# Optimization experiments

Measured on AMD Instinct MI355X. Metric: run time of the kernel, lower is better.

Reference implementation:

```python
import jax, jax.numpy as jnp
import numpy as np
import math

D_MODEL = 1024
N_HEADS = 16
D_HEAD = D_MODEL // N_HEADS

def setup_inputs() -> dict:
    key = jax.random.key(0)
    k1, k2, k3 = jax.random.split(key, 3)
    x = jax.random.normal(k1, (4, 2048, D_MODEL), dtype=jnp.float32)
    # torch Linear weights are [out, in]; kept in that layout, applied as x @ W.T
    s = 1.0 / math.sqrt(D_MODEL)
    W_qkv = jax.random.uniform(k2, (3 * D_MODEL, D_MODEL), jnp.float32, -s, s)
    W_proj = jax.random.uniform(k3, (D_MODEL, D_MODEL), jnp.float32, -s, s)
    return {"x": x, "W_qkv": W_qkv, "W_proj": W_proj}

def reference(x, W_qkv, W_proj):
    B, T, d = x.shape
    qkv = x @ W_qkv.T  # [B,T,3d]
    q, k, v = jnp.split(qkv, 3, axis=-1)
    def split(t):
        return t.reshape(B, T, N_HEADS, D_HEAD).transpose(0, 2, 1, 3)  # [B,H,T,Dh]
    q, k, v = split(q), split(k), split(v)
    scores = jnp.einsum('bhqd,bhkd->bhqk', q, k) / math.sqrt(D_HEAD)
    mask = jnp.tril(jnp.ones((T, T), dtype=bool))
    scores = jnp.where(mask, scores, -jnp.inf)
    attn = jax.nn.softmax(scores, axis=-1)
    out = jnp.einsum('bhqk,bhkd->bhqd', attn, v)  # [B,H,T,Dh]
    out = out.transpose(0, 2, 1, 3).reshape(B, T, d)
    return out @ W_proj.T
```

## Files before the change

kernel.cpp:

```cpp
#include <hip/hip_runtime.h>
#include <hip/hip_bf16.h>
#include <math.h>

typedef __attribute__((ext_vector_type(8))) short short8;
typedef __attribute__((ext_vector_type(4))) float f32x4;
typedef __attribute__((ext_vector_type(16))) float f32x16;
typedef __attribute__((ext_vector_type(2))) unsigned uint2v;
typedef __attribute__((ext_vector_type(4))) unsigned uint4v;

#define B_  4
#define T_  2048
#define DM  1024
#define NH  16
#define DH  64
#define BH  (B_*NH)
#define M_  (B_*T_)

#define QSCALE 0.18033688011112042f

static __device__ __forceinline__ short f2bf(float f) {
  unsigned u = __float_as_uint(f);
  unsigned r = (u + 0x7fff + ((u >> 16) & 1)) >> 16;
  return (short)r;
}

static __device__ __forceinline__ unsigned cvtpk(float lo, float hi) {
  unsigned r;
  asm("v_cvt_pk_bf16_f32 %0, %1, %2" : "=v"(r) : "v"(lo), "v"(hi));
  return r;
}

static __device__ __forceinline__ float expasm(float x) {
  float r;
  asm("v_exp_f32 %0, %1" : "=v"(r) : "v"(x));
  return r;
}

static __device__ __forceinline__ void gload_lds16(const void* g, void* l) {
  __builtin_amdgcn_global_load_lds((const __attribute__((address_space(1))) void*)g,
                                   (__attribute__((address_space(3))) void*)l, 16, 0, 0);
}

__global__ void k_cvt3(const float4* __restrict__ x, const float4* __restrict__ wq,
                       const float4* __restrict__ wp, ushort4* __restrict__ ox,
                       ushort4* __restrict__ oq, ushort4* __restrict__ op) {
  const int n1 = M_ * DM / 4, n2 = 3 * DM * DM / 4, n3 = DM * DM / 4;
  int i = blockIdx.x * 256 + threadIdx.x;
  const float4* src;
  ushort4* dst;
  int j = i;
  if (i < n1) { src = x; dst = ox; }
  else if (i < n1 + n2) { src = wq; dst = oq; j = i - n1; }
  else if (i < n1 + n2 + n3) { src = wp; dst = op; j = i - n1 - n2; }
  else return;
  float4 v = src[j];
  ushort4 o;
  o.x = (ushort)f2bf(v.x); o.y = (ushort)f2bf(v.y);
  o.z = (ushort)f2bf(v.z); o.w = (ushort)f2bf(v.w);
  dst[j] = o;
}

#define GEMM_STAGE(SRCA, SRCB, dA, dB, m0_, n0_, k0_)                          \
  {                                                                            \
    _Pragma("unroll")                                                          \
    for (int i = 0; i < 4; ++i) {                                              \
      int lin = i * 256 + tid;                                                 \
      int row = lin >> 3, pseg = lin & 7;                                      \
      int gseg = pseg ^ (row & 7);                                             \
      gload_lds16(&SRCA[(size_t)((m0_) + row) * DM + (k0_) + gseg * 8],        \
                  &(dA)[lin * 8]);                                             \
    }                                                                          \
    _Pragma("unroll")                                                          \
    for (int i = 0; i < 4; ++i) {                                              \
      int lin = i * 256 + tid;                                                 \
      int row = lin >> 3, pseg = lin & 7;                                      \
      int gseg = pseg ^ (row & 7);                                             \
      gload_lds16(&SRCB[(size_t)((n0_) + row) * DM + (k0_) + gseg * 8],        \
                  &(dB)[lin * 8]);                                             \
    }                                                                          \
  }

#define GEMM_COMPUTE(pA, pB)                                                   \
  {                                                                            \
    _Pragma("unroll")                                                          \
    for (int kk = 0; kk < 2; ++kk) {                                           \
      short8 aF[4], bF[4];                                                     \
      _Pragma("unroll")                                                        \
      for (int m = 0; m < 4; ++m)                                              \
        aF[m] = *(const short8*)&(pA)[(wr * 64 + m * 16 + fr) * 64 +           \
                                      (((kk * 4 + fq) ^ (fr & 7)) * 8)];       \
      _Pragma("unroll")                                                        \
      for (int n = 0; n < 4; ++n)                                              \
        bF[n] = *(const short8*)&(pB)[(wc * 64 + n * 16 + fr) * 64 +           \
                                      (((kk * 4 + fq) ^ (fr & 7)) * 8)];       \
      __builtin_amdgcn_s_setprio(1);                                           \
      _Pragma("unroll")                                                        \
      for (int m = 0; m < 4; ++m)                                              \
        _Pragma("unroll")                                                      \
        for (int n = 0; n < 4; ++n)                                            \
          acc[m][n] = __builtin_amdgcn_mfma_f32_16x16x32_bf16(aF[m], bF[n],    \
                                                              acc[m][n], 0, 0, 0); \
      __builtin_amdgcn_s_setprio(0);                                           \
    }                                                                          \
  }

#define GEMM_KLOOP(SRCA, SRCB, m0_, n0_)                                       \
  GEMM_STAGE(SRCA, SRCB, sA0, sB0, m0_, n0_, 0);                               \
  {                                                                            \
    _Pragma("unroll 1")                                                        \
    for (int t = 0; t < 16; ++t) {                                             \
      short* pA = (t & 1) ? sA1 : sA0;                                         \
      short* pB = (t & 1) ? sB1 : sB0;                                         \
      if (t < 15) {                                                            \
        short* nA = (t & 1) ? sA0 : sA1;                                       \
        short* nB = (t & 1) ? sB0 : sB1;                                       \
        GEMM_STAGE(SRCA, SRCB, nA, nB, m0_, n0_, (t + 1) * 64);                \
        asm volatile("s_waitcnt vmcnt(8)" ::: "memory");                       \
      } else {                                                                 \
        asm volatile("s_waitcnt vmcnt(0)" ::: "memory");                       \
      }                                                                        \
      __builtin_amdgcn_s_barrier();                                            \
      __builtin_amdgcn_sched_barrier(0);                                       \
      GEMM_COMPUTE(pA, pB);                                                    \
      asm volatile("" ::: "memory");                                           \
      __builtin_amdgcn_s_barrier();                                            \
    }                                                                          \
  }

__global__ __launch_bounds__(256, 2) void k_gemm_qkv(
    const short* __restrict__ A,
    const short* __restrict__ W,
    short* __restrict__ Qb, short* __restrict__ Kb, short* __restrict__ Vtb) {
  const int tid = threadIdx.x;
  const int w = tid >> 6, l = tid & 63;
  const int wr = w >> 1, wc = w & 1;
  const int fq = l >> 4, fr = l & 15;
  const int m0 = blockIdx.x * 128;
  const int n0 = blockIdx.y * 128;

  __shared__ short lds[32768];
  short* sA0 = lds;
  short* sA1 = lds + 8192;
  short* sB0 = lds + 16384;
  short* sB1 = lds + 24576;

  f32x4 acc[4][4] = {};
  GEMM_KLOOP(A, W, m0, n0);
  __syncthreads();

  short* sE = lds;
  const int part = n0 >> 10;
  const int b = m0 >> 11, tloc = m0 & 2047;

  if (part < 2) {
    const float sc = part ? 1.0f : QSCALE;
#pragma unroll
    for (int m = 0; m < 4; ++m)
#pragma unroll
      for (int n = 0; n < 4; ++n)
#pragma unroll
        for (int j = 0; j < 4; ++j)
          sE[(wr * 64 + m * 16 + fq * 4 + j) * 136 + wc * 64 + n * 16 + fr] =
              f2bf(acc[m][n][j] * sc);
    __syncthreads();
    short* dst = part ? Kb : Qb;
    const int h0 = (n0 & 1023) >> 6;
#pragma unroll
    for (int v = 0; v < 8; ++v) {
      int vid = v * 256 + tid;
      int row = vid >> 4, seg = vid & 15;
      short8 val = *(const short8*)&sE[row * 136 + seg * 8];
      int h = h0 + (seg >> 3), dh0 = (seg & 7) * 8;
      *(short8*)&dst[(((size_t)(b * NH + h) * T_ + tloc + row)) * DH + dh0] = val;
    }
  } else {
#pragma unroll
    for (int m = 0; m < 4; ++m)
#pragma unroll
      for (int n = 0; n < 4; ++n) {
        uint2v pk;
        pk[0] = cvtpk(acc[m][n][0], acc[m][n][1]);
        pk[1] = cvtpk(acc[m][n][2], acc[m][n][3]);
        *(uint2v*)&sE[(wc * 64 + n * 16 + fr) * 136 + wr * 64 + m * 16 + fq * 4] = pk;
      }
    __syncthreads();
    const int h0 = (n0 & 1023) >> 6;
#pragma unroll
    for (int v = 0; v < 8; ++v) {
      int vid = v * 256 + tid;
      int col = vid >> 4, seg = vid & 15;
      short8 val = *(const short8*)&sE[col * 136 + seg * 8];
      int h = h0 + (col >> 6), dh = col & 63;
      *(short8*)&Vtb[(((size_t)(b * NH + h) * DH + dh)) * T_ + tloc + seg * 8] = val;
    }
  }
}

__global__ __launch_bounds__(256, 2) void k_gemm_proj(
    const short* __restrict__ A,
    const short* __restrict__ W,
    float* __restrict__ C) {
  const int tid = threadIdx.x;
  const int w = tid >> 6, l = tid & 63;
  const int wr = w >> 1, wc = w & 1;
  const int fq = l >> 4, fr = l & 15;
  const int m0 = blockIdx.x * 128;
  const int n0 = blockIdx.y * 128;

  __shared__ short lds[32768];
  short* sA0 = lds;
  short* sA1 = lds + 8192;
  short* sB0 = lds + 16384;
  short* sB1 = lds + 24576;

  f32x4 acc[4][4] = {};
  GEMM_KLOOP(A, W, m0, n0);

#pragma unroll
  for (int m = 0; m < 4; ++m) {
    int row0 = m0 + wr * 64 + m * 16 + fq * 4;
#pragma unroll
    for (int n = 0; n < 4; ++n) {
      int col = n0 + wc * 64 + n * 16 + fr;
#pragma unroll
      for (int j = 0; j < 4; ++j)
        C[(size_t)(row0 + j) * DM + col] = acc[m][n][j];
    }
  }
}

__global__ __launch_bounds__(256, 4) void k_attn5(
    const short* __restrict__ Qb,
    const short* __restrict__ Kb,
    const short* __restrict__ Vtb,
    short* __restrict__ Ob) {
  const int tid = threadIdx.x;
  const int w = tid >> 6, l = tid & 63;
  const int lq = l & 31, hi = l >> 5;
  const int id = blockIdx.x;
  const int g = id >> 3;
  const int r_ = g >> 3, a_ = r_ & 3, b_ = r_ >> 2;
  const int qt = 15 - (4 * b_ + ((a_ + b_) & 3));
  const int bh = (id & 7) + 8 * (g & 7);
  const int b = bh >> 4, h = bh & 15;

  __shared__ short lds[16384];
  short* sK = lds;
  short* sVt = lds + 8192;

  auto STAGE = [&](int buf, int kt) {
#pragma unroll
    for (int i = 0; i < 2; ++i) {
      int lin = i * 256 + tid;
      int row = lin >> 3, pseg = lin & 7;
      int gseg = pseg ^ (row & 7);
      gload_lds16(&Kb[((size_t)bh * T_ + kt * 64 + row) * DH + gseg * 8],
                  &sK[buf * 4096 + lin * 8]);
    }
#pragma unroll
    for (int i = 0; i < 2; ++i) {
      int lin = i * 256 + tid;
      int row = lin >> 3, pseg = lin & 7;
      int gseg = pseg ^ (row & 7);
      gload_lds16(&Vtb[((size_t)bh * DH + row) * T_ + kt * 64 + gseg * 8],
                  &sVt[buf * 4096 + lin * 8]);
    }
  };

  const int nkt = 2 * qt + 2;
  const int q0 = qt * 128 + w * 32;
  const int qg = q0 + lq;

  short8 qf[4];
#pragma unroll
  for (int c = 0; c < 4; ++c)
    qf[c] = *(const short8*)&Qb[((size_t)bh * T_ + qg) * DH + c * 16 + hi * 8];
  asm volatile("s_waitcnt vmcnt(0)" ::: "memory");

  float lsum = 0.f;
  f32x16 oacc[2] = {};

  auto COMPUTE = [&](int kt, const int koff) {
    f32x16 a0 = {}, a1 = {};
    __builtin_amdgcn_s_setprio(1);
#pragma unroll
    for (int c = 0; c < 4; ++c) {
      short8 kf0 = *(const short8*)&sK[koff + (lq) * 64 + (((2 * c + hi) ^ (lq & 7)) * 8)];
      short8 kf1 = *(const short8*)&sK[koff + (32 + lq) * 64 + (((2 * c + hi) ^ (lq & 7)) * 8)];
      a0 = __builtin_amdgcn_mfma_f32_32x32x16_bf16(kf0, qf[c], a0, 0, 0, 0);
      a1 = __builtin_amdgcn_mfma_f32_32x32x16_bf16(kf1, qf[c], a1, 0, 0, 0);
    }
    __builtin_amdgcn_s_setprio(0);

    if (kt * 64 + 63 > q0) {
#pragma unroll
      for (int r = 0; r < 16; ++r) {
        int kg0 = kt * 64 + (r & 3) + 8 * (r >> 2) + 4 * hi;
        if (kg0 > qg) a0[r] = -1e30f;
        if (kg0 + 32 > qg) a1[r] = -1e30f;
      }
    }

#pragma unroll
    for (int r = 0; r < 16; ++r) {
      a0[r] = expasm(a0[r]);
      a1[r] = expasm(a1[r]);
    }
    {
      float t[8];
#pragma unroll
      for (int i = 0; i < 8; ++i) t[i] = (a0[2 * i] + a0[2 * i + 1]) + (a1[2 * i] + a1[2 * i + 1]);
      float u0 = (t[0] + t[1]) + (t[2] + t[3]);
      float u1 = (t[4] + t[5]) + (t[6] + t[7]);
      lsum += u0 + u1;
    }

    short8 pb[4];
#pragma unroll
    for (int st = 0; st < 2; ++st) {
      const f32x16& P = st ? a1 : a0;
      unsigned x0 = cvtpk(P[0], P[1]);
      unsigned x1 = cvtpk(P[2], P[3]);
      unsigned y0 = cvtpk(P[4], P[5]);
      unsigned y1 = cvtpk(P[6], P[7]);
      uint2v r0 = __builtin_amdgcn_permlane32_swap(x0, y0, false, false);
      uint2v r1 = __builtin_amdgcn_permlane32_swap(x1, y1, false, false);
      unsigned x2 = cvtpk(P[8], P[9]);
      unsigned x3 = cvtpk(P[10], P[11]);
      unsigned y2 = cvtpk(P[12], P[13]);
      unsigned y3 = cvtpk(P[14], P[15]);
      uint2v r2 = __builtin_amdgcn_permlane32_swap(x2, y2, false, false);
      uint2v r3 = __builtin_amdgcn_permlane32_swap(x3, y3, false, false);
      uint4v ta, tb;
      ta[0] = r0[0]; ta[1] = r1[0]; ta[2] = r0[1]; ta[3] = r1[1];
      tb[0] = r2[0]; tb[1] = r3[0]; tb[2] = r2[1]; tb[3] = r3[1];
      pb[st * 2 + 0] = __builtin_bit_cast(short8, ta);
      pb[st * 2 + 1] = __builtin_bit_cast(short8, tb);
    }

    __builtin_amdgcn_s_setprio(1);
#pragma unroll
    for (int dt = 0; dt < 2; ++dt) {
#pragma unroll
      for (int c = 0; c < 4; ++c) {
        short8 vf = *(const short8*)&sVt[koff + (dt * 32 + lq) * 64 +
                                         (((2 * c + hi) ^ (lq & 7)) * 8)];
        oacc[dt] = __builtin_amdgcn_mfma_f32_32x32x16_bf16(vf, pb[c], oacc[dt], 0, 0, 0);
      }
    }
    __builtin_amdgcn_s_setprio(0);
  };

  STAGE(0, 0);
  int kt = 0;
  while (true) {
    if (kt + 1 < nkt) {
      STAGE(1, kt + 1);
      asm volatile("s_waitcnt vmcnt(4)" ::: "memory");
    } else {
      asm volatile("s_waitcnt vmcnt(0)" ::: "memory");
    }
    __builtin_amdgcn_s_barrier();
    __builtin_amdgcn_sched_barrier(0);
    COMPUTE(kt, 0);
    __builtin_amdgcn_s_barrier();
    if (++kt == nkt) break;

    if (kt + 1 < nkt) {
      STAGE(0, kt + 1);
      asm volatile("s_waitcnt vmcnt(4)" ::: "memory");
    } else {
      asm volatile("s_waitcnt vmcnt(0)" ::: "memory");
    }
    __builtin_amdgcn_s_barrier();
    __builtin_amdgcn_sched_barrier(0);
    COMPUTE(kt, 4096);
    __builtin_amdgcn_s_barrier();
    if (++kt == nkt) break;
  }

  lsum += __shfl_xor(lsum, 32);
  __syncthreads();
  short* sO = lds + w * 2304;
  float inv = 1.0f / lsum;
#pragma unroll
  for (int dt = 0; dt < 2; ++dt)
#pragma unroll
    for (int r = 0; r < 16; r += 2) {
      int dl = dt * 32 + (r & 3) + 8 * (r >> 2) + 4 * hi;
      unsigned pk2 = cvtpk(oacc[dt][r] * inv, oacc[dt][r + 1] * inv);
      *(unsigned*)&sO[lq * 72 + dl] = pk2;
    }
  __syncthreads();
  {
    int qr = l >> 1, hf = l & 1;
    const int tg = qt * 128 + w * 32 + qr;
#pragma unroll
    for (int ss = 0; ss < 4; ++ss) {
      short8 v = *(const short8*)&sO[qr * 72 + hf * 32 + ss * 8];
      *(short8*)&Ob[((size_t)(b * T_) + tg) * DM + h * 64 + hf * 32 + ss * 8] = v;
    }
  }
}

extern "C" void kernel_launch(void* const* d_in, const int* in_sizes, int n_in,
                              void* d_out, int out_size, void* d_ws, size_t ws_size,
                              hipStream_t stream) {
  const float* x     = (const float*)d_in[0];
  const float* Wqkv  = (const float*)d_in[1];
  const float* Wproj = (const float*)d_in[2];
  float* out = (float*)d_out;

  short* ws = (short*)d_ws;
  short* xbf   = ws;
  short* wqkvb = xbf + (size_t)M_ * DM;
  short* wprjb = wqkvb + (size_t)3 * DM * DM;
  short* Qb    = wprjb + (size_t)DM * DM;
  short* Kb    = Qb + (size_t)BH * T_ * DH;
  short* Vtb   = Kb + (size_t)BH * T_ * DH;
  short* Ob    = Vtb + (size_t)BH * T_ * DH;

  const int ncv = (M_ * DM + 3 * DM * DM + DM * DM) / 4;
  k_cvt3<<<(ncv + 255) / 256, 256, 0, stream>>>(
      (const float4*)x, (const float4*)Wqkv, (const float4*)Wproj,
      (ushort4*)xbf, (ushort4*)wqkvb, (ushort4*)wprjb);

  k_gemm_qkv<<<dim3(M_ / 128, 3 * DM / 128), 256, 0, stream>>>(xbf, wqkvb, Qb, Kb, Vtb);
  k_attn5<<<1024, 256, 0, stream>>>(Qb, Kb, Vtb, Ob);
  k_gemm_proj<<<dim3(M_ / 128, DM / 128), 256, 0, stream>>>(Ob, wprjb, out);
}
```

Before: 161.2 us.

## Split long causal query tiles across two KV halves and merge partials

Query tiles with long causal key ranges are split into two blocks, each processing half the key tiles and writing unnormalized bf16 partial outputs and row sums to scratch. A new merge kernel adds the partials and normalizes them into the output. A lookup table orders the work units so heavy units are scheduled first, and launch bounds are raised to allow more resident blocks. This aims to even out per-block work and reduce tail imbalance, at the cost of an extra kernel launch, extra global traffic and bf16 rounding of the partials.

```diff
diff --git a/kernel.cpp b/kernel.cpp
--- a/kernel.cpp
+++ b/kernel.cpp
@@ -24,6 +24,10 @@
   return (short)r;
 }
 
+static __device__ __forceinline__ float bf2f(short s) {
+  return __uint_as_float(((unsigned)(unsigned short)s) << 16);
+}
+
 static __device__ __forceinline__ unsigned cvtpk(float lo, float hi) {
   unsigned r;
   asm("v_cvt_pk_bf16_f32 %0, %1, %2" : "=v"(r) : "v"(lo), "v"(hi));
@@ -40,6 +44,11 @@
   __builtin_amdgcn_global_load_lds((const __attribute__((address_space(1))) void*)g,
                                    (__attribute__((address_space(3))) void*)l, 16, 0, 0);
 }
+
+static __device__ const signed char U_QT[24] =
+    {7, 15, 15, 14, 14, 6, 13, 13, 12, 12, 5, 11, 11, 10, 10, 4, 9, 9, 8, 8, 3, 2, 1, 0};
+static __device__ const signed char U_HALF[24] =
+    {-1, 0, 1, 0, 1, -1, 0, 1, 0, 1, -1, 0, 1, 0, 1, -1, 0, 1, 0, 1, -1, -1, -1, -1};
 
 __global__ void k_cvt3(const float4* __restrict__ x, const float4* __restrict__ wq,
                        const float4* __restrict__ wp, ushort4* __restrict__ ox,
@@ -229,19 +238,24 @@
   }
 }
 
-__global__ __launch_bounds__(256, 4) void k_attn5(
+__global__ __launch_bounds__(256, 5) void k_attn6(
     const short* __restrict__ Qb,
     const short* __restrict__ Kb,
     const short* __restrict__ Vtb,
-    short* __restrict__ Ob) {
+    short* __restrict__ Ob,
+    short* __restrict__ Pbuf,
+    float* __restrict__ Lbuf) {
   const int tid = threadIdx.x;
   const int w = tid >> 6, l = tid & 63;
   const int lq = l & 31, hi = l >> 5;
   const int id = blockIdx.x;
-  const int g = id >> 3;
-  const int r_ = g >> 3, a_ = r_ & 3, b_ = r_ >> 2;
-  const int qt = 15 - (4 * b_ + ((a_ + b_) & 3));
-  const int bh = (id & 7) + 8 * (g & 7);
+  const int u = id >> 6;
+  const int bh = id & 63;
+  const int qt = U_QT[u];
+  const int half = U_HALF[u];
+  const bool split = half >= 0;
+  const int nloc = split ? (qt + 1) : (2 * qt + 2);
+  const int kbeg = split ? half * (qt + 1) : 0;
   const int b = bh >> 4, h = bh & 15;
 
   __shared__ short lds[16384];
@@ -267,7 +281,6 @@
     }
   };
 
-  const int nkt = 2 * qt + 2;
   const int q0 = qt * 128 + w * 32;
   const int qg = q0 + lq;
 
@@ -351,38 +364,38 @@
     __builtin_amdgcn_s_setprio(0);
   };
 
-  STAGE(0, 0);
-  int kt = 0;
+  STAGE(0, kbeg);
+  int t = 0;
   while (true) {
-    if (kt + 1 < nkt) {
-      STAGE(1, kt + 1);
+    if (t + 1 < nloc) {
+      STAGE(1, kbeg + t + 1);
       asm volatile("s_waitcnt vmcnt(4)" ::: "memory");
     } else {
       asm volatile("s_waitcnt vmcnt(0)" ::: "memory");
     }
     __builtin_amdgcn_s_barrier();
     __builtin_amdgcn_sched_barrier(0);
-    COMPUTE(kt, 0);
+    COMPUTE(kbeg + t, 0);
     __builtin_amdgcn_s_barrier();
-    if (++kt == nkt) break;
-
-    if (kt + 1 < nkt) {
-      STAGE(0, kt + 1);
+    if (++t == nloc) break;
+
+    if (t + 1 < nloc) {
+      STAGE(0, kbeg + t + 1);
       asm volatile("s_waitcnt vmcnt(4)" ::: "memory");
     } else {
       asm volatile("s_waitcnt vmcnt(0)" ::: "memory");
     }
     __builtin_amdgcn_s_barrier();
     __builtin_amdgcn_sched_barrier(0);
-    COMPUTE(kt, 4096);
+    COMPUTE(kbeg + t, 4096);
     __builtin_amdgcn_s_barrier();
-    if (++kt == nkt) break;
+    if (++t == nloc) break;
   }
 
   lsum += __shfl_xor(lsum, 32);
   __syncthreads();
   short* sO = lds + w * 2304;
-  float inv = 1.0f / lsum;
+  float inv = split ? 1.0f : (1.0f / lsum);
 #pragma unroll
   for (int dt = 0; dt < 2; ++dt)
 #pragma unroll
@@ -392,7 +405,7 @@
       *(unsigned*)&sO[lq * 72 + dl] = pk2;
     }
   __syncthreads();
-  {
+  if (!split) {
     int qr = l >> 1, hf = l & 1;
     const int tg = qt * 128 + w * 32 + qr;
 #pragma unroll
@@ -400,6 +413,45 @@
       short8 v = *(const short8*)&sO[qr * 72 + hf * 32 + ss * 8];
       *(short8*)&Ob[((size_t)(b * T_) + tg) * DM + h * 64 + hf * 32 + ss * 8] = v;
     }
+  } else {
+    const int pid = (bh * 8 + (qt - 8)) * 2 + half;
+    int qr = l >> 1, hf = l & 1;
+    const int row = w * 32 + qr;
+#pragma unroll
+    for (int ss = 0; ss < 4; ++ss) {
+      short8 v = *(const short8*)&sO[qr * 72 + hf * 32 + ss * 8];
+      *(short8*)&Pbuf[(size_t)pid * 8192 + row * 64 + hf * 32 + ss * 8] = v;
+    }
+    if (hi == 0) Lbuf[pid * 128 + w * 32 + lq] = lsum;
+  }
+}
+
+__global__ __launch_bounds__(256) void k_merge(
+    const short* __restrict__ P, const float* __restrict__ L,
+    short* __restrict__ Ob) {
+  const int sid = blockIdx.x;
+  const int bh = sid >> 3, q8 = sid & 7;
+  const int qt = 8 + q8;
+  const int b = bh >> 4, h = bh & 15;
+  const int pid0 = (bh * 8 + q8) * 2;
+  const short* p0 = P + (size_t)pid0 * 8192;
+  const short* p1 = p0 + 8192;
+  const float* l0 = L + pid0 * 128;
+  const float* l1 = l0 + 128;
+  const int tid = threadIdx.x;
+#pragma unroll
+  for (int v = 0; v < 4; ++v) {
+    int idx = v * 256 + tid;
+    int row = idx >> 3, seg = idx & 7;
+    short8 a = *(const short8*)&p0[row * 64 + seg * 8];
+    short8 c = *(const short8*)&p1[row * 64 + seg * 8];
+    float inv = 1.0f / (l0[row] + l1[row]);
+    short8 o;
+#pragma unroll
+    for (int i = 0; i < 8; ++i)
+      o[i] = f2bf((bf2f(a[i]) + bf2f(c[i])) * inv);
+    const int tg = qt * 128 + row;
+    *(short8*)&Ob[((size_t)(b * T_) + tg) * DM + h * 64 + seg * 8] = o;
   }
 }
 
@@ -419,6 +471,8 @@
   short* Kb    = Qb + (size_t)BH * T_ * DH;
   short* Vtb   = Kb + (size_t)BH * T_ * DH;
   short* Ob    = Vtb + (size_t)BH * T_ * DH;
+  short* Pbuf  = xbf;
+  float* Lbuf  = (float*)wqkvb;
 
   const int ncv = (M_ * DM + 3 * DM * DM + DM * DM) / 4;
   k_cvt3<<<(ncv + 255) / 256, 256, 0, stream>>>(
@@ -426,6 +480,7 @@
       (ushort4*)xbf, (ushort4*)wqkvb, (ushort4*)wprjb);
 
   k_gemm_qkv<<<dim3(M_ / 128, 3 * DM / 128), 256, 0, stream>>>(xbf, wqkvb, Qb, Kb, Vtb);
-  k_attn5<<<1024, 256, 0, stream>>>(Qb, Kb, Vtb, Ob);
+  k_attn6<<<1536, 256, 0, stream>>>(Qb, Kb, Vtb, Ob, Pbuf, Lbuf);
+  k_merge<<<512, 256, 0, stream>>>(Pbuf, Lbuf, Ob);
   k_gemm_proj<<<dim3(M_ / 128, DM / 128), 256, 0, stream>>>(Ob, wprjb, out);
 }
```

Measured after the change: 207.2 us. 28.6% more time.

## Process two query tiles per attention block to share staged K/V tiles

Applied to the files above, without the earlier changes.

The attention kernel now gives each block two 128-row query sub-tiles, 256 rows in total, instead of one. Each staged K/V LDS tile is reused by both sub-tiles, with per-sub-tile causal skipping. This halves the grid to 512 blocks, lowers the launch-bounds occupancy hint to 2, and adds a new block-to-(qt, bh) ordering. The goal is to cut K/V global and LDS staging traffic, at the cost of more registers, fewer blocks, and possible load imbalance across CUs.

```diff
diff --git a/kernel.cpp b/kernel.cpp
--- a/kernel.cpp
+++ b/kernel.cpp
@@ -229,7 +229,7 @@
   }
 }
 
-__global__ __launch_bounds__(256, 4) void k_attn5(
+__global__ __launch_bounds__(256, 2) void k_attn7(
     const short* __restrict__ Qb,
     const short* __restrict__ Kb,
     const short* __restrict__ Vtb,
@@ -238,10 +238,9 @@
   const int w = tid >> 6, l = tid & 63;
   const int lq = l & 31, hi = l >> 5;
   const int id = blockIdx.x;
-  const int g = id >> 3;
-  const int r_ = g >> 3, a_ = r_ & 3, b_ = r_ >> 2;
-  const int qt = 15 - (4 * b_ + ((a_ + b_) & 3));
-  const int bh = (id & 7) + 8 * (g & 7);
+  const int u = id >> 6;
+  const int bh = id & 63;
+  const int qt = (u < 4) ? (7 - u) : (u - 4);
   const int b = bh >> 4, h = bh & 15;
 
   __shared__ short lds[16384];
@@ -267,20 +266,23 @@
     }
   };
 
-  const int nkt = 2 * qt + 2;
-  const int q0 = qt * 128 + w * 32;
-  const int qg = q0 + lq;
-
-  short8 qf[4];
-#pragma unroll
-  for (int c = 0; c < 4; ++c)
-    qf[c] = *(const short8*)&Qb[((size_t)bh * T_ + qg) * DH + c * 16 + hi * 8];
+  const int nkt = 4 * qt + 4;
+  const int q00 = qt * 256 + w * 32;
+  const int q01 = q00 + 128;
+
+  short8 qf0[4], qf1[4];
+#pragma unroll
+  for (int c = 0; c < 4; ++c) {
+    qf0[c] = *(const short8*)&Qb[((size_t)bh * T_ + q00 + lq) * DH + c * 16 + hi * 8];
+    qf1[c] = *(const short8*)&Qb[((size_t)bh * T_ + q01 + lq) * DH + c * 16 + hi * 8];
+  }
   asm volatile("s_waitcnt vmcnt(0)" ::: "memory");
 
-  float lsum = 0.f;
-  f32x16 oacc[2] = {};
-
-  auto COMPUTE = [&](int kt, const int koff) {
+  float ls0 = 0.f, ls1 = 0.f;
+  f32x16 oa0[2] = {}, oa1[2] = {};
+
+  auto CSUB = [&](int kt, const int koff, const short8 (&qf)[4],
+                  f32x16 (&oacc)[2], float& lsum, int q0s) {
     f32x16 a0 = {}, a1 = {};
     __builtin_amdgcn_s_setprio(1);
 #pragma unroll
@@ -292,7 +294,8 @@
     }
     __builtin_amdgcn_s_setprio(0);
 
-    if (kt * 64 + 63 > q0) {
+    if (kt * 64 + 63 > q0s) {
+      const int qg = q0s + lq;
 #pragma unroll
       for (int r = 0; r < 16; ++r) {
         int kg0 = kt * 64 + (r & 3) + 8 * (r >> 2) + 4 * hi;
@@ -309,7 +312,8 @@
     {
       float t[8];
 #pragma unroll
-      for (int i = 0; i < 8; ++i) t[i] = (a0[2 * i] + a0[2 * i + 1]) + (a1[2 * i] + a1[2 * i + 1]);
+      for (int i = 0; i < 8; ++i)
+        t[i] = (a0[2 * i] + a0[2 * i + 1]) + (a1[2 * i] + a1[2 * i + 1]);
       float u0 = (t[0] + t[1]) + (t[2] + t[3]);
       float u1 = (t[4] + t[5]) + (t[6] + t[7]);
       lsum += u0 + u1;
@@ -352,49 +356,73 @@
   };
 
   STAGE(0, 0);
-  int kt = 0;
+  int t = 0;
   while (true) {
-    if (kt + 1 < nkt) {
-      STAGE(1, kt + 1);
+    if (t + 1 < nkt) {
+      STAGE(1, t + 1);
       asm volatile("s_waitcnt vmcnt(4)" ::: "memory");
     } else {
       asm volatile("s_waitcnt vmcnt(0)" ::: "memory");
     }
     __builtin_amdgcn_s_barrier();
     __builtin_amdgcn_sched_barrier(0);
-    COMPUTE(kt, 0);
+    if (t * 64 <= q00 + 31) CSUB(t, 0, qf0, oa0, ls0, q00);
+    if (t * 64 <= q01 + 31) CSUB(t, 0, qf1, oa1, ls1, q01);
     __builtin_amdgcn_s_barrier();
-    if (++kt == nkt) break;
-
-    if (kt + 1 < nkt) {
-      STAGE(0, kt + 1);
+    if (++t == nkt) break;
+
+    if (t + 1 < nkt) {
+      STAGE(0, t + 1);
       asm volatile("s_waitcnt vmcnt(4)" ::: "memory");
     } else {
       asm volatile("s_waitcnt vmcnt(0)" ::: "memory");
     }
     __builtin_amdgcn_s_barrier();
     __builtin_amdgcn_sched_barrier(0);
-    COMPUTE(kt, 4096);
+    if (t * 64 <= q00 + 31) CSUB(t, 4096, qf0, oa0, ls0, q00);
+    if (t * 64 <= q01 + 31) CSUB(t, 4096, qf1, oa1, ls1, q01);
     __builtin_amdgcn_s_barrier();
-    if (++kt == nkt) break;
-  }
-
-  lsum += __shfl_xor(lsum, 32);
+    if (++t == nkt) break;
+  }
+
+  ls0 += __shfl_xor(ls0, 32);
+  ls1 += __shfl_xor(ls1, 32);
   __syncthreads();
   short* sO = lds + w * 2304;
-  float inv = 1.0f / lsum;
-#pragma unroll
-  for (int dt = 0; dt < 2; ++dt)
-#pragma unroll
-    for (int r = 0; r < 16; r += 2) {
-      int dl = dt * 32 + (r & 3) + 8 * (r >> 2) + 4 * hi;
-      unsigned pk2 = cvtpk(oacc[dt][r] * inv, oacc[dt][r + 1] * inv);
-      *(unsigned*)&sO[lq * 72 + dl] = pk2;
-    }
-  __syncthreads();
+  const int qr = l >> 1, hf = l & 1;
+
   {
-    int qr = l >> 1, hf = l & 1;
-    const int tg = qt * 128 + w * 32 + qr;
+    float inv = 1.0f / ls0;
+#pragma unroll
+    for (int dt = 0; dt < 2; ++dt)
+#pragma unroll
+      for (int r = 0; r < 16; r += 2) {
+        int dl = dt * 32 + (r & 3) + 8 * (r >> 2) + 4 * hi;
+        *(unsigned*)&sO[lq * 72 + dl] = cvtpk(oa0[dt][r] * inv, oa0[dt][r + 1] * inv);
+      }
+    asm volatile("s_waitcnt lgkmcnt(0)" ::: "memory");
+    __builtin_amdgcn_sched_barrier(0);
+    const int tg = q00 - w * 32 + w * 32 + qr;
+#pragma unroll
+    for (int ss = 0; ss < 4; ++ss) {
+      short8 v = *(const short8*)&sO[qr * 72 + hf * 32 + ss * 8];
+      *(short8*)&Ob[((size_t)(b * T_) + tg) * DM + h * 64 + hf * 32 + ss * 8] = v;
+    }
+    asm volatile("s_waitcnt lgkmcnt(0)" ::: "memory");
+    __builtin_amdgcn_sched_barrier(0);
+  }
+  {
+    float inv = 1.0f / ls1;
+#pragma unroll
+    for (int dt = 0; dt < 2; ++dt)
+#pragma unroll
+      for (int r = 0; r < 16; r += 2) {
+        int dl = dt * 32 + (r & 3) + 8 * (r >> 2) + 4 * hi;
+        *(unsigned*)&sO[lq * 72 + dl] = cvtpk(oa1[dt][r] * inv, oa1[dt][r + 1] * inv);
+      }
+    asm volatile("s_waitcnt lgkmcnt(0)" ::: "memory");
+    __builtin_amdgcn_sched_barrier(0);
+    const int tg = q01 - w * 32 + w * 32 + qr;
 #pragma unroll
     for (int ss = 0; ss < 4; ++ss) {
       short8 v = *(const short8*)&sO[qr * 72 + hf * 32 + ss * 8];
@@ -426,6 +454,6 @@
       (ushort4*)xbf, (ushort4*)wqkvb, (ushort4*)wprjb);
 
   k_gemm_qkv<<<dim3(M_ / 128, 3 * DM / 128), 256, 0, stream>>>(xbf, wqkvb, Qb, Kb, Vtb);
-  k_attn5<<<1024, 256, 0, stream>>>(Qb, Kb, Vtb, Ob);
+  k_attn7<<<512, 256, 0, stream>>>(Qb, Kb, Vtb, Ob);
   k_gemm_proj<<<dim3(M_ / 128, DM / 128), 256, 0, stream>>>(Ob, wprjb, out);
 }
```

Result: faster. 141.4 us (-12.2%).

## Enlarge attention blocks to 8 waves sharing K/V tiles across 256 query rows

Applied to the files above, without the earlier changes.

Doubles the attention block to 512 threads covering 256 query rows, so each staged K/V tile is reused by twice as many waves and global K/V traffic per query is halved. Waves skip compute on fully masked key tiles, the grid ordering of query tiles is remapped, and the output epilogue replaces a block barrier with a per-wave LDS wait. The tradeoff is intra-block imbalance from causal masking, since early waves idle at barriers, plus fewer and larger blocks for scheduling.

```diff
diff --git a/kernel.cpp b/kernel.cpp
--- a/kernel.cpp
+++ b/kernel.cpp
@@ -229,7 +229,7 @@
   }
 }
 
-__global__ __launch_bounds__(256, 4) void k_attn5(
+__global__ __launch_bounds__(512, 4) void k_attn11(
     const short* __restrict__ Qb,
     const short* __restrict__ Kb,
     const short* __restrict__ Vtb,
@@ -238,37 +238,26 @@
   const int w = tid >> 6, l = tid & 63;
   const int lq = l & 31, hi = l >> 5;
   const int id = blockIdx.x;
-  const int g = id >> 3;
-  const int r_ = g >> 3, a_ = r_ & 3, b_ = r_ >> 2;
-  const int qt = 15 - (4 * b_ + ((a_ + b_) & 3));
-  const int bh = (id & 7) + 8 * (g & 7);
+  const int x = id >> 6;
+  const int qt = (x < 4) ? (7 - x) : (x - 4);
+  const int bh = id & 63;
   const int b = bh >> 4, h = bh & 15;
 
-  __shared__ short lds[16384];
+  __shared__ short lds[18432];
   short* sK = lds;
   short* sVt = lds + 8192;
 
   auto STAGE = [&](int buf, int kt) {
-#pragma unroll
-    for (int i = 0; i < 2; ++i) {
-      int lin = i * 256 + tid;
-      int row = lin >> 3, pseg = lin & 7;
-      int gseg = pseg ^ (row & 7);
-      gload_lds16(&Kb[((size_t)bh * T_ + kt * 64 + row) * DH + gseg * 8],
-                  &sK[buf * 4096 + lin * 8]);
-    }
-#pragma unroll
-    for (int i = 0; i < 2; ++i) {
-      int lin = i * 256 + tid;
-      int row = lin >> 3, pseg = lin & 7;
-      int gseg = pseg ^ (row & 7);
-      gload_lds16(&Vtb[((size_t)bh * DH + row) * T_ + kt * 64 + gseg * 8],
-                  &sVt[buf * 4096 + lin * 8]);
-    }
+    int row = tid >> 3, pseg = tid & 7;
+    int gseg = pseg ^ (row & 7);
+    gload_lds16(&Kb[((size_t)bh * T_ + kt * 64 + row) * DH + gseg * 8],
+                &sK[buf * 4096 + tid * 8]);
+    gload_lds16(&Vtb[((size_t)bh * DH + row) * T_ + kt * 64 + gseg * 8],
+                &sVt[buf * 4096 + tid * 8]);
   };
 
-  const int nkt = 2 * qt + 2;
-  const int q0 = qt * 128 + w * 32;
+  const int nkt = 4 * qt + 4;
+  const int q0 = qt * 256 + w * 32;
   const int qg = q0 + lq;
 
   short8 qf[4];
@@ -280,7 +269,7 @@
   float lsum = 0.f;
   f32x16 oacc[2] = {};
 
-  auto COMPUTE = [&](int kt, const int koff) {
+  auto CSUB = [&](int kt, const int koff) {
     f32x16 a0 = {}, a1 = {};
     __builtin_amdgcn_s_setprio(1);
 #pragma unroll
@@ -309,7 +298,8 @@
     {
       float t[8];
 #pragma unroll
-      for (int i = 0; i < 8; ++i) t[i] = (a0[2 * i] + a0[2 * i + 1]) + (a1[2 * i] + a1[2 * i + 1]);
+      for (int i = 0; i < 8; ++i)
+        t[i] = (a0[2 * i] + a0[2 * i + 1]) + (a1[2 * i] + a1[2 * i + 1]);
       float u0 = (t[0] + t[1]) + (t[2] + t[3]);
       float u1 = (t[4] + t[5]) + (t[6] + t[7]);
       lsum += u0 + u1;
@@ -352,31 +342,31 @@
   };
 
   STAGE(0, 0);
-  int kt = 0;
+  int t = 0;
   while (true) {
-    if (kt + 1 < nkt) {
-      STAGE(1, kt + 1);
-      asm volatile("s_waitcnt vmcnt(4)" ::: "memory");
+    if (t + 1 < nkt) {
+      STAGE(1, t + 1);
+      asm volatile("s_waitcnt vmcnt(2)" ::: "memory");
     } else {
       asm volatile("s_waitcnt vmcnt(0)" ::: "memory");
     }
     __builtin_amdgcn_s_barrier();
     __builtin_amdgcn_sched_barrier(0);
-    COMPUTE(kt, 0);
+    if (t * 64 <= q0 + 31) CSUB(t, 0);
     __builtin_amdgcn_s_barrier();
-    if (++kt == nkt) break;
-
-    if (kt + 1 < nkt) {
-      STAGE(0, kt + 1);
-      asm volatile("s_waitcnt vmcnt(4)" ::: "memory");
+    if (++t == nkt) break;
+
+    if (t + 1 < nkt) {
+      STAGE(0, t + 1);
+      asm volatile("s_waitcnt vmcnt(2)" ::: "memory");
     } else {
       asm volatile("s_waitcnt vmcnt(0)" ::: "memory");
     }
     __builtin_amdgcn_s_barrier();
     __builtin_amdgcn_sched_barrier(0);
-    COMPUTE(kt, 4096);
+    if (t * 64 <= q0 + 31) CSUB(t, 4096);
     __builtin_amdgcn_s_barrier();
-    if (++kt == nkt) break;
+    if (++t == nkt) break;
   }
 
   lsum += __shfl_xor(lsum, 32);
@@ -388,13 +378,13 @@
 #pragma unroll
     for (int r = 0; r < 16; r += 2) {
       int dl = dt * 32 + (r & 3) + 8 * (r >> 2) + 4 * hi;
-      unsigned pk2 = cvtpk(oacc[dt][r] * inv, oacc[dt][r + 1] * inv);
-      *(unsigned*)&sO[lq * 72 + dl] = pk2;
-    }
-  __syncthreads();
+      *(unsigned*)&sO[lq * 72 + dl] = cvtpk(oacc[dt][r] * inv, oacc[dt][r + 1] * inv);
+    }
+  asm volatile("s_waitcnt lgkmcnt(0)" ::: "memory");
+  __builtin_amdgcn_sched_barrier(0);
   {
     int qr = l >> 1, hf = l & 1;
-    const int tg = qt * 128 + w * 32 + qr;
+    const int tg = q0 + qr;
 #pragma unroll
     for (int ss = 0; ss < 4; ++ss) {
       short8 v = *(const short8*)&sO[qr * 72 + hf * 32 + ss * 8];
@@ -426,6 +416,6 @@
       (ushort4*)xbf, (ushort4*)wqkvb, (ushort4*)wprjb);
 
   k_gemm_qkv<<<dim3(M_ / 128, 3 * DM / 128), 256, 0, stream>>>(xbf, wqkvb, Qb, Kb, Vtb);
-  k_attn5<<<1024, 256, 0, stream>>>(Qb, Kb, Vtb, Ob);
+  k_attn11<<<512, 512, 0, stream>>>(Qb, Kb, Vtb, Ob);
   k_gemm_proj<<<dim3(M_ / 128, DM / 128), 256, 0, stream>>>(Ob, wprjb, out);
 }
```

Result: faster. 136.0 us (-15.6%).
